# Kernel optimization log

Hardware: AMD Instinct MI355X
Metric: run time of the kernel (lower is better)

The kernel has to match this reference:

```python
import jax, jax.numpy as jnp
import numpy as np

# static config (matches init_kwargs)
E = 1280          # n_embed
L = 4             # n_layer
NH = 16           # n_heads
D = E // NH       # head_dim = 80
M = 5120          # n_mlp
O = 2048          # n_output_embed
MS = 2            # spatial_merge_size
NGPS = 48         # sqrt(num_position_embeddings)
GRID_T, GRID_H, GRID_W = 1, 32, 32
N_IMG = 2
SPP = GRID_T * GRID_H * GRID_W   # 1024 tokens per image
S = N_IMG * SPP                  # 2048 total tokens
H4 = E * MS * MS                 # merger hidden = 5120
IN_PATCH = 3 * 2 * 16 * 16       # 1536
DS_IDX = [1, 2]


def _ln(x, w, b, eps=1e-6):
    m = x.mean(-1, keepdims=True)
    v = ((x - m) ** 2).mean(-1, keepdims=True)
    return (x - m) / jnp.sqrt(v + eps) * w + b


def _pos_embed_interp(pos_emb):
    # bilinear interpolation of the 48x48 learned grid to GRID_HxGRID_W, per image
    hi = jnp.linspace(0.0, NGPS - 1.0, GRID_H)
    wi = jnp.linspace(0.0, NGPS - 1.0, GRID_W)
    hf = hi.astype(jnp.int32); wf = wi.astype(jnp.int32)
    hc = jnp.minimum(hf + 1, NGPS - 1); wc = jnp.minimum(wf + 1, NGPS - 1)
    dh = hi - hf; dw = wi - wf
    idx = [(hf[:, None] * NGPS + wf[None]).ravel(), (hf[:, None] * NGPS + wc[None]).ravel(),
           (hc[:, None] * NGPS + wf[None]).ravel(), (hc[:, None] * NGPS + wc[None]).ravel()]
    wts = [((1 - dh)[:, None] * (1 - dw)[None]).ravel(), ((1 - dh)[:, None] * dw[None]).ravel(),
           (dh[:, None] * (1 - dw)[None]).ravel(), (dh[:, None] * dw[None]).ravel()]
    pe = sum(pos_emb[i] * w[:, None] for i, w in zip(idx, wts))  # [h*w, E]
    pe = jnp.tile(pe, (GRID_T, 1))
    # spatial-merge permutation: (t, h/m, m, w/m, m) -> (t, h/m, w/m, m, m)
    pe = pe.reshape(GRID_T, GRID_H // MS, MS, GRID_W // MS, MS, E).transpose(0, 1, 3, 2, 4, 5).reshape(-1, E)
    return jnp.tile(pe, (N_IMG, 1))  # [S, E]


def _rotary_freqs():
    dim = D // 2  # VisionRotaryEmbedding dim = 40
    inv = 1.0 / (10000.0 ** (jnp.arange(0, dim, 2, dtype=jnp.float32) / dim))  # [D//4]
    hp = jnp.broadcast_to(jnp.arange(GRID_H)[:, None], (GRID_H, GRID_W))
    hp = hp.reshape(GRID_H // MS, MS, GRID_W // MS, MS).transpose(0, 2, 1, 3).ravel()
    wp = jnp.broadcast_to(jnp.arange(GRID_W)[None, :], (GRID_H, GRID_W))
    wp = wp.reshape(GRID_H // MS, MS, GRID_W // MS, MS).transpose(0, 2, 1, 3).ravel()
    pos = jnp.stack([hp, wp], -1)            # [h*w, 2]
    pos = jnp.tile(pos, (GRID_T, 1))
    pos = jnp.tile(pos, (N_IMG, 1))          # [S, 2]
    table = jnp.arange(max(GRID_H, GRID_W), dtype=jnp.float32)[:, None] * inv[None]  # [G, D//4]
    return table[pos].reshape(S, -1)         # [S, D//2] (h-freqs || w-freqs)


def _rope(t, cos, sin):
    # t: [S, NH, D]; cos/sin: [S, 1, D]; applied in float32 as in the source
    t1, t2 = jnp.split(t, 2, axis=-1)
    rot = jnp.concatenate([-t2, t1], -1)
    return (t.astype(jnp.float32) * cos + rot.astype(jnp.float32) * sin).astype(t.dtype)


def _attn(x, qkv_w, qkv_b, pw, pb, cos, sin, mask):
    qkv = (x @ qkv_w.T + qkv_b).reshape(S, 3, NH, D)
    q, k, v = qkv[:, 0], qkv[:, 1], qkv[:, 2]
    q = _rope(q, cos, sin)
    k = _rope(k, cos, sin)
    scores = jnp.einsum('shd,thd->hst', q, k) / np.sqrt(D).astype(np.float32) + mask
    p = jax.nn.softmax(scores.astype(jnp.float32), axis=-1).astype(q.dtype)
    o = jnp.einsum('hst,thd->shd', p, v).reshape(S, E)
    return o @ pw.T + pb


def _merger(x, ln_w, ln_b, f1w, f1b, f2w, f2b, post):
    if post:
        x = _ln(x.reshape(-1, H4), ln_w, ln_b)
    else:
        x = _ln(x, ln_w, ln_b).reshape(-1, H4)
    h = jax.nn.gelu(x @ f1w.T + f1b, approximate=False)  # nn.GELU() exact
    return h @ f2w.T + f2b


def setup_inputs() -> dict:
    key = jax.random.key(0)
    ks = iter(jax.random.split(key, 24))
    n = lambda s: jax.random.normal(next(ks), s, dtype=jnp.float32) * 0.02
    return {
        'x': jax.random.normal(next(ks), (S, IN_PATCH), dtype=jnp.float32),
        'patch_w': n((E, IN_PATCH)), 'patch_b': jnp.zeros((E,), jnp.float32),
        'pos_emb': n((NGPS * NGPS, E)),
        'ln1_w': jnp.ones((L, E), jnp.float32), 'ln1_b': jnp.zeros((L, E), jnp.float32),
        'ln2_w': jnp.ones((L, E), jnp.float32), 'ln2_b': jnp.zeros((L, E), jnp.float32),
        'qkv_w': n((L, 3 * E, E)), 'qkv_b': jnp.zeros((L, 3 * E), jnp.float32),
        'attn_proj_w': n((L, E, E)), 'attn_proj_b': jnp.zeros((L, E), jnp.float32),
        'fc1_w': n((L, M, E)), 'fc1_b': jnp.zeros((L, M), jnp.float32),
        'fc2_w': n((L, E, M)), 'fc2_b': jnp.zeros((L, E), jnp.float32),
        'm_ln_w': jnp.ones((E,), jnp.float32), 'm_ln_b': jnp.zeros((E,), jnp.float32),
        'm_fc1_w': n((H4, H4)), 'm_fc1_b': jnp.zeros((H4,), jnp.float32),
        'm_fc2_w': n((O, H4)), 'm_fc2_b': jnp.zeros((O,), jnp.float32),
        'ds_ln_w': jnp.ones((2, H4), jnp.float32), 'ds_ln_b': jnp.zeros((2, H4), jnp.float32),
        'ds_fc1_w': n((2, H4, H4)), 'ds_fc1_b': jnp.zeros((2, H4), jnp.float32),
        'ds_fc2_w': n((2, O, H4)), 'ds_fc2_b': jnp.zeros((2, O), jnp.float32),
    }


def reference(x, patch_w, patch_b, pos_emb, ln1_w, ln1_b, ln2_w, ln2_b,
              qkv_w, qkv_b, attn_proj_w, attn_proj_b, fc1_w, fc1_b, fc2_w, fc2_b,
              m_ln_w, m_ln_b, m_fc1_w, m_fc1_b, m_fc2_w, m_fc2_b,
              ds_ln_w, ds_ln_b, ds_fc1_w, ds_fc1_b, ds_fc2_w, ds_fc2_b):
    # patch embed (Conv3d with kernel==stride == per-patch linear)
    h = x @ patch_w.T + patch_b                      # [S, E]
    h = h + _pos_embed_interp(pos_emb)
    freqs = _rotary_freqs()                          # [S, D//2]
    cos = jnp.concatenate([jnp.cos(freqs)] * 2, -1)[:, None, :]  # [S,1,D]
    sin = jnp.concatenate([jnp.sin(freqs)] * 2, -1)[:, None, :]
    img = jnp.arange(S) // SPP                       # cu_seqlens block-diagonal mask
    mask = jnp.where(img[:, None] == img[None, :], 0.0, jnp.finfo(jnp.float32).min)
    ds_feats = []
    for l in range(L):
        h = h + _attn(_ln(h, ln1_w[l], ln1_b[l]), qkv_w[l], qkv_b[l],
                      attn_proj_w[l], attn_proj_b[l], cos, sin, mask)
        hn = _ln(h, ln2_w[l], ln2_b[l])
        h = h + (jax.nn.gelu(hn @ fc1_w[l].T + fc1_b[l], approximate=True) @ fc2_w[l].T + fc2_b[l])
        if l in DS_IDX:
            j = DS_IDX.index(l)
            ds_feats.append(_merger(h, ds_ln_w[j], ds_ln_b[j], ds_fc1_w[j], ds_fc1_b[j],
                                    ds_fc2_w[j], ds_fc2_b[j], post=True))
    main = _merger(h, m_ln_w, m_ln_b, m_fc1_w, m_fc1_b, m_fc2_w, m_fc2_b, post=False)
    return jnp.stack([main] + ds_feats, 0)           # [3, S//4, O]
```

## Files before the change

kernel.cpp:

```cpp
#include <hip/hip_runtime.h>
#include <hip/hip_bf16.h>
#include <cstdio>
#include <cstdint>

#define E_    1280
#define L_    4
#define NH_   16
#define D_    80
#define DP_   96
#define MLP_  5120
#define O_    2048
#define S_    2048
#define H4_   5120
#define INP_  1536

typedef __attribute__((ext_vector_type(4))) float f32x4;
typedef __attribute__((ext_vector_type(8))) short short8v;
typedef __attribute__((ext_vector_type(4))) short short4v;

__device__ __forceinline__ short f2bf(float f){
  uint32_t u = __float_as_uint(f);
  uint32_t r = (u + 0x7FFFu + ((u >> 16) & 1u)) >> 16;
  return (short)r;
}
__device__ __forceinline__ float bf2f(short s){
  return __uint_as_float(((uint32_t)(uint16_t)s) << 16);
}
__device__ __forceinline__ float gelu_tanh(float x){
  return 0.5f*x*(1.f + tanhf(0.7978845608028654f*(x + 0.044715f*x*x*x)));
}
__device__ __forceinline__ float gelu_erf(float x){
  return 0.5f*x*(1.f + erff(x*0.7071067811865476f));
}
__device__ __forceinline__ void token_hw(int t, int& hc, int& wc){
  hc = ((t>>1)&1) + ((t>>6)<<1);
  wc = (t&1)      + (((t>>2)&15)<<1);
}

__device__ __forceinline__ void gload16(const short* g, short* l){
  __builtin_amdgcn_global_load_lds((const __attribute__((address_space(1))) void*)g,
                                   (__attribute__((address_space(3))) void*)l, 16, 0, 0);
}

__global__ __launch_bounds__(256)
void cvt_k(const float* __restrict__ src, short* __restrict__ dst, long long n)
{
  const long long stride = (long long)gridDim.x*256*8;
  for (long long i = ((long long)blockIdx.x*256 + threadIdx.x)*8; i < n; i += stride){
    if (i + 8 <= n){
      float4 v0 = *(const float4*)(src+i);
      float4 v1 = *(const float4*)(src+i+4);
      short8v w;
      w[0]=f2bf(v0.x); w[1]=f2bf(v0.y); w[2]=f2bf(v0.z); w[3]=f2bf(v0.w);
      w[4]=f2bf(v1.x); w[5]=f2bf(v1.y); w[6]=f2bf(v1.z); w[7]=f2bf(v1.w);
      *(short8v*)(dst+i) = w;
    } else {
      for (long long j=i;j<n;j++) dst[j] = f2bf(src[j]);
    }
  }
}

struct Gemm2P {
  const short* A; const short* B; void* C;
  const float* bias;
  float* part;
  int lda, ldb, ldc, M, N, K;
  float scale;
  long long aOffH, aOffI, bOffH, bOffI, cOffH, cOffI;
  int nImg, kSplit;
};

template<int EPI, bool RES, bool CF32, bool SPLIT>
__global__ __launch_bounds__(256)
void gemm2_k(Gemm2P p)
{
  __shared__ short As[3][4096];
  __shared__ short Bs[3][4096];

  int z = blockIdx.z, ks = 0;
  if constexpr (SPLIT){ ks = z % p.kSplit; z /= p.kSplit; }
  const int hI = z / p.nImg, iI = z % p.nImg;
  const long long aB = (long long)hI*p.aOffH + (long long)iI*p.aOffI;
  const long long bB = (long long)hI*p.bOffH + (long long)iI*p.bOffI;
  const long long cB = (long long)hI*p.cOffH + (long long)iI*p.cOffI;

  const int nwg = gridDim.x*gridDim.y;
  const int orig = blockIdx.y*gridDim.x + blockIdx.x;
  const int q8 = nwg >> 3, r8 = nwg & 7;
  const int xcd = orig & 7, oidx = orig >> 3;
  const int wg = (xcd < r8 ? xcd*(q8+1) : r8*(q8+1) + (xcd-r8)*q8) + oidx;
  const int nt = wg % gridDim.x, mt = wg / gridDim.x;

  const int tid = threadIdx.x, lane = tid & 63, wv = tid >> 6;

  const int sr = lane >> 2;
  const int sc = (lane & 3) * 8;
  const int Kp  = SPLIT ? p.K / p.kSplit : p.K;
  const int kBeg = SPLIT ? ks * Kp : 0;
  int ra0 = mt*128 + (wv*2+0)*16 + sr; if (ra0 >= p.M) ra0 = p.M-1;
  int ra1 = mt*128 + (wv*2+1)*16 + sr; if (ra1 >= p.M) ra1 = p.M-1;
  int rb0 = nt*128 + (wv*2+0)*16 + sr; if (rb0 >= p.N) rb0 = p.N-1;
  int rb1 = nt*128 + (wv*2+1)*16 + sr; if (rb1 >= p.N) rb1 = p.N-1;
  const short* pa0 = p.A + aB + (long long)ra0*p.lda + sc + kBeg;
  const short* pa1 = p.A + aB + (long long)ra1*p.lda + sc + kBeg;
  const short* pb0 = p.B + bB + (long long)rb0*p.ldb + sc + kBeg;
  const short* pb1 = p.B + bB + (long long)rb1*p.ldb + sc + kBeg;
  const int so0 = (wv*2+0)*512;
  const int so1 = (wv*2+1)*512;

  const int fr = lane & 15, fo = (lane >> 4) * 8;
  const int wr = (wv >> 1) * 64, wc = (wv & 1) * 64;

  f32x4 acc[4][4] = {};

  auto stage = [&](int buf, int t){
    const int k0 = t << 5;
    gload16(pa0 + k0, &As[buf][so0]);
    gload16(pa1 + k0, &As[buf][so1]);
    gload16(pb0 + k0, &Bs[buf][so0]);
    gload16(pb1 + k0, &Bs[buf][so1]);
  };

  const int ntile = Kp >> 5;
  stage(0, 0);
  if (ntile > 1) stage(1, 1);
  for (int t = 0; t < ntile; t++){
    const int cur = t % 3;
    if (t + 1 < ntile) { asm volatile("s_waitcnt vmcnt(4)" ::: "memory"); }
    else               { asm volatile("s_waitcnt vmcnt(0)" ::: "memory"); }
    __builtin_amdgcn_s_barrier();
    asm volatile("" ::: "memory");
    short8v a[4], b[4];
    #pragma unroll
    for (int i=0;i<4;i++){
      a[i] = *(const short8v*)&As[cur][(wr + i*16 + fr)*32 + fo];
      b[i] = *(const short8v*)&Bs[cur][(wc + i*16 + fr)*32 + fo];
    }
    #pragma unroll
    for (int i=0;i<4;i++)
      #pragma unroll
      for (int j=0;j<4;j++)
        acc[i][j] = __builtin_amdgcn_mfma_f32_16x16x32_bf16(a[i], b[j], acc[i][j], 0, 0, 0);
    if (t + 2 < ntile) stage((t+2)%3, t+2);
  }

  #pragma unroll
  for (int i=0;i<4;i++){
    #pragma unroll
    for (int j=0;j<4;j++){
      #pragma unroll
      for (int r=0;r<4;r++){
        const int row = mt*128 + wr + i*16 + (lane>>4)*4 + r;
        const int col = nt*128 + wc + j*16 + fr;
        if (row < p.M && col < p.N){
          float v = acc[i][j][r];
          if constexpr (SPLIT){
            p.part[((long long)ks*p.M + row)*p.N + col] = v;
          } else {
            if (p.bias) v += p.bias[col];
            if constexpr (EPI==1) v = gelu_tanh(v);
            if constexpr (EPI==2) v = gelu_erf(v);
            if constexpr (EPI==3) v *= p.scale;
            const long long off = cB + (long long)row*p.ldc + col;
            if constexpr (RES)  v += ((const float*)p.C)[off];
            if constexpr (CF32) ((float*)p.C)[off] = v;
            else                ((short*)p.C)[off] = f2bf(v);
          }
        }
      }
    }
  }
}

template<int EPI, bool RES, bool CF32>
__global__ __launch_bounds__(256)
void reduce_k(const float* __restrict__ part, int kSplit, long long MN, int N,
              const float* __restrict__ bias, void* __restrict__ C)
{
  const long long i = ((long long)blockIdx.x*256 + threadIdx.x)*4;
  if (i >= MN) return;
  float4 s = *(const float4*)(part + i);
  for (int ks = 1; ks < kSplit; ks++){
    const float4 v = *(const float4*)(part + (long long)ks*MN + i);
    s.x += v.x; s.y += v.y; s.z += v.z; s.w += v.w;
  }
  if (bias){
    const int col = (int)(i % N);
    const float4 b = *(const float4*)(bias + col);
    s.x += b.x; s.y += b.y; s.z += b.z; s.w += b.w;
  }
  if constexpr (EPI==1){ s.x=gelu_tanh(s.x); s.y=gelu_tanh(s.y); s.z=gelu_tanh(s.z); s.w=gelu_tanh(s.w); }
  if constexpr (EPI==2){ s.x=gelu_erf(s.x);  s.y=gelu_erf(s.y);  s.z=gelu_erf(s.z);  s.w=gelu_erf(s.w); }
  if constexpr (RES){
    const float4 r = *(const float4*)((const float*)C + i);
    s.x += r.x; s.y += r.y; s.z += r.z; s.w += r.w;
  }
  if constexpr (CF32){
    *(float4*)((float*)C + i) = s;
  } else {
    short4v o; o[0]=f2bf(s.x); o[1]=f2bf(s.y); o[2]=f2bf(s.z); o[3]=f2bf(s.w);
    *(short4v*)((short*)C + i) = o;
  }
}

__global__ __launch_bounds__(256)
void fattn_k(const short* __restrict__ qh, const short* __restrict__ kh,
             const short* __restrict__ vt, short* __restrict__ o2)
{
  __shared__ short Ks[2][13312];
  __shared__ short Vs[2][12288];
  __shared__ short Ps[17408];

  const int qt = blockIdx.x, h = blockIdx.y, img = blockIdx.z;
  const int tid = threadIdx.x, lane = tid & 63, wv = tid >> 6;
  const int fr = lane & 15, fo = (lane >> 4) * 8, g = lane >> 4;
  const int wr = wv * 32;

  const short* qp = qh + ((long long)h*S_ + img*1024 + qt*128)*DP_;
  const short* kp = kh + ((long long)h*S_ + img*1024)*DP_;
  const short* vp = vt + ((long long)(h*2 + img))*80*1024;

  short8v q[2][3];
  #pragma unroll
  for (int i=0;i<2;i++)
    #pragma unroll
    for (int t3=0;t3<3;t3++)
      q[i][t3] = *(const short8v*)(qp + (long long)(wr + i*16 + fr)*DP_ + t3*32 + fo);

  int rK[7], cK[7], rV[6], cV[6];
  #pragma unroll
  for (int it=0; it<7; it++){
    const int o = it*4096 + tid*16;
    int r = o / 208, c = o % 208;
    if (c >= 192) c = 0;
    rK[it] = r; cK[it] = c >> 1;
  }
  #pragma unroll
  for (int it=0; it<6; it++){
    const int o = it*4096 + tid*16;
    int r = o / 304, c = o % 304;
    if (r >= 80){ r = 0; c = 0; }
    if (c >= 256) c = 0;
    rV[it] = r; cV[it] = c >> 1;
  }

  auto stage = [&](int b, int t){
    #pragma unroll
    for (int it=0; it<7; it++)
      if (it*4 + wv < 26)
        gload16(kp + (long long)(t*128 + rK[it])*DP_ + cK[it], &Ks[b][it*2048 + wv*512]);
    #pragma unroll
    for (int it=0; it<6; it++)
      gload16(vp + (long long)rV[it]*1024 + t*128 + cV[it], &Vs[b][it*2048 + wv*512]);
  };

  float m_[2][4], l_[2][4];
  f32x4 ao[2][5] = {};
  #pragma unroll
  for (int i=0;i<2;i++)
    #pragma unroll
    for (int r=0;r<4;r++){ m_[i][r] = -3.0e38f; l_[i][r] = 0.f; }

  stage(0, 0);
  __syncthreads();

  for (int t = 0; t < 8; t++){
    const int b = t & 1;
    if (t < 7) stage(b^1, t+1);

    f32x4 sc[2][8] = {};
    #pragma unroll
    for (int j=0;j<8;j++){
      #pragma unroll
      for (int t3=0;t3<3;t3++){
        const short8v kb = *(const short8v*)&Ks[b][(j*16+fr)*104 + t3*32 + fo];
        sc[0][j] = __builtin_amdgcn_mfma_f32_16x16x32_bf16(q[0][t3], kb, sc[0][j], 0,0,0);
        sc[1][j] = __builtin_amdgcn_mfma_f32_16x16x32_bf16(q[1][t3], kb, sc[1][j], 0,0,0);
      }
    }
    #pragma unroll
    for (int i=0;i<2;i++)
      #pragma unroll
      for (int j=0;j<8;j++)
        sc[i][j] *= 0.11180339887498949f;

    #pragma unroll
    for (int i=0;i<2;i++){
      #pragma unroll
      for (int r=0;r<4;r++){
        float mx = sc[i][0][r];
        #pragma unroll
        for (int j=1;j<8;j++) mx = fmaxf(mx, sc[i][j][r]);
        mx = fmaxf(mx, __shfl_xor(mx, 1, 64));
        mx = fmaxf(mx, __shfl_xor(mx, 2, 64));
        mx = fmaxf(mx, __shfl_xor(mx, 4, 64));
        mx = fmaxf(mx, __shfl_xor(mx, 8, 64));
        const float mn = fmaxf(m_[i][r], mx);
        const float al = __expf(m_[i][r] - mn);
        float ts = 0.f;
        #pragma unroll
        for (int j=0;j<8;j++){
          const float pv = __expf(sc[i][j][r] - mn);
          sc[i][j][r] = pv;
          ts += pv;
        }
        ts += __shfl_xor(ts, 1, 64);
        ts += __shfl_xor(ts, 2, 64);
        ts += __shfl_xor(ts, 4, 64);
        ts += __shfl_xor(ts, 8, 64);
        l_[i][r] = l_[i][r]*al + ts;
        m_[i][r] = mn;
        #pragma unroll
        for (int n=0;n<5;n++) ao[i][n][r] *= al;
        const int row = wr + i*16 + g*4 + r;
        #pragma unroll
        for (int j=0;j<8;j++) Ps[row*136 + j*16 + fr] = f2bf(sc[i][j][r]);
      }
    }

    #pragma unroll
    for (int t4=0;t4<4;t4++){
      short8v pa0 = *(const short8v*)&Ps[(wr + 0  + fr)*136 + t4*32 + fo];
      short8v pa1 = *(const short8v*)&Ps[(wr + 16 + fr)*136 + t4*32 + fo];
      #pragma unroll
      for (int n=0;n<5;n++){
        const short8v vb = *(const short8v*)&Vs[b][(n*16+fr)*152 + t4*32 + fo];
        ao[0][n] = __builtin_amdgcn_mfma_f32_16x16x32_bf16(pa0, vb, ao[0][n], 0,0,0);
        ao[1][n] = __builtin_amdgcn_mfma_f32_16x16x32_bf16(pa1, vb, ao[1][n], 0,0,0);
      }
    }
    __syncthreads();
  }

  short* op = o2 + ((long long)(img*1024 + qt*128))*E_ + h*80;
  #pragma unroll
  for (int i=0;i<2;i++){
    #pragma unroll
    for (int r=0;r<4;r++){
      const float inv = 1.f / l_[i][r];
      const int row = wr + i*16 + g*4 + r;
      #pragma unroll
      for (int n=0;n<5;n++)
        op[(long long)row*E_ + n*16 + fr] = f2bf(ao[i][n][r] * inv);
    }
  }
}

__global__ __launch_bounds__(256)
void ln_k(const float* __restrict__ X, const float* __restrict__ g, const float* __restrict__ bta,
          short* __restrict__ Y, int Cn)
{
  __shared__ float red[8];
  const int row = blockIdx.x;
  const float* x = X + (long long)row*Cn;
  short* y = Y + (long long)row*Cn;
  float s = 0.f, sq = 0.f;
  for (int c = threadIdx.x*4; c < Cn; c += 1024){
    float4 v = *(const float4*)(x + c);
    s  += v.x+v.y+v.z+v.w;
    sq += v.x*v.x+v.y*v.y+v.z*v.z+v.w*v.w;
  }
  #pragma unroll
  for (int m=32;m;m>>=1){ s += __shfl_xor(s,m,64); sq += __shfl_xor(sq,m,64); }
  const int wv = threadIdx.x>>6, lane = threadIdx.x&63;
  if (lane==0){ red[wv]=s; red[4+wv]=sq; }
  __syncthreads();
  s  = red[0]+red[1]+red[2]+red[3];
  sq = red[4]+red[5]+red[6]+red[7];
  const float mean = s / (float)Cn;
  const float var  = sq / (float)Cn - mean*mean;
  const float rs   = rsqrtf(var + 1e-6f);
  for (int c = threadIdx.x*4; c < Cn; c += 1024){
    float4 v  = *(const float4*)(x + c);
    float4 gw = *(const float4*)(g + c);
    float4 bw = *(const float4*)(bta + c);
    short4v o;
    o[0] = f2bf((v.x-mean)*rs*gw.x + bw.x);
    o[1] = f2bf((v.y-mean)*rs*gw.y + bw.y);
    o[2] = f2bf((v.z-mean)*rs*gw.z + bw.z);
    o[3] = f2bf((v.w-mean)*rs*gw.w + bw.w);
    *(short4v*)(y + c) = o;
  }
}

__global__ __launch_bounds__(256)
void rope_k(const short* __restrict__ qkv, short* __restrict__ qh,
            short* __restrict__ kh, short* __restrict__ vt)
{
  const int idx = blockIdx.x*256 + threadIdx.x;
  if (idx >= S_*NH_*40) return;
  const int d0 = idx % 40;
  const int h  = (idx / 40) % NH_;
  const int s  = idx / (40*NH_);
  const int t  = s & 1023, img = s >> 10;
  int hc, wc; token_hw(t, hc, wc);
  const int j  = d0 % 20;
  const float invf = exp2f(-0.66438561897747f * (float)j);
  const float pos  = (float)((d0 < 20) ? hc : wc);
  float sn, cs; sincosf(pos * invf, &sn, &cs);
  const short* base = qkv + (long long)s*3840 + h*80;
  const float q1 = bf2f(base[d0]),      q2 = bf2f(base[d0+40]);
  const float k1 = bf2f(base[1280+d0]), k2 = bf2f(base[1280+d0+40]);
  const long long qo = ((long long)h*S_ + s)*DP_;
  qh[qo + d0]    = f2bf(q1*cs - q2*sn);
  qh[qo + d0+40] = f2bf(q2*cs + q1*sn);
  kh[qo + d0]    = f2bf(k1*cs - k2*sn);
  kh[qo + d0+40] = f2bf(k2*cs + k1*sn);
  if (d0 < 16){ qh[qo + 80 + d0] = 0; kh[qo + 80 + d0] = 0; }
  const long long vo = (((long long)h*2 + img)*80)*1024 + t;
  vt[vo + (long long)d0*1024]      = base[2560+d0];
  vt[vo + (long long)(d0+40)*1024] = base[2560+d0+40];
}

__global__ __launch_bounds__(256)
void posadd_k(float* __restrict__ h, const float* __restrict__ pe)
{
  const int idx = blockIdx.x*256 + threadIdx.x;
  if (idx >= S_*(E_/4)) return;
  const int c4 = idx % (E_/4), s = idx / (E_/4);
  const int e = c4*4;
  const int t = s & 1023;
  int hc, wc; token_hw(t, hc, wc);
  const float hi = (float)hc * (47.f/31.f);
  const float wi = (float)wc * (47.f/31.f);
  int hf = (int)hi; float dh = hi - (float)hf; int h2 = min(hf+1, 47);
  int wf = (int)wi; float dw = wi - (float)wf; int w2 = min(wf+1, 47);
  const float w00=(1.f-dh)*(1.f-dw), w01=(1.f-dh)*dw, w10=dh*(1.f-dw), w11=dh*dw;
  const float4 a = *(const float4*)(pe + ((long long)(hf*48+wf))*E_ + e);
  const float4 b = *(const float4*)(pe + ((long long)(hf*48+w2))*E_ + e);
  const float4 c = *(const float4*)(pe + ((long long)(h2*48+wf))*E_ + e);
  const float4 d = *(const float4*)(pe + ((long long)(h2*48+w2))*E_ + e);
  float* out = h + (long long)s*E_ + e;
  float4 o = *(float4*)out;
  o.x += w00*a.x + w01*b.x + w10*c.x + w11*d.x;
  o.y += w00*a.y + w01*b.y + w10*c.y + w11*d.y;
  o.z += w00*a.z + w01*b.z + w10*c.z + w11*d.z;
  o.w += w00*a.w + w01*b.w + w10*c.w + w11*d.w;
  *(float4*)out = o;
}

static Gemm2P mk(const short* A, const short* B, void* C, const float* bias,
                 int lda, int ldb, int ldc, int M, int N, int K, float scale = 1.f)
{
  Gemm2P p{}; p.A=A; p.B=B; p.C=C; p.bias=bias; p.part=nullptr;
  p.lda=lda; p.ldb=ldb; p.ldc=ldc; p.M=M; p.N=N; p.K=K; p.scale=scale;
  p.aOffH=p.aOffI=p.bOffH=p.bOffI=p.cOffH=p.cOffI=0; p.nImg=1; p.kSplit=1;
  return p;
}

extern "C" void kernel_launch(void* const* d_in, const int* in_sizes, int n_in,
                              void* d_out, int out_size, void* d_ws, size_t ws_size,
                              hipStream_t stream)
{
  const float* x           = (const float*)d_in[0];
  const float* patch_w     = (const float*)d_in[1];
  const float* patch_b     = (const float*)d_in[2];
  const float* pos_emb     = (const float*)d_in[3];
  const float* ln1_w       = (const float*)d_in[4];
  const float* ln1_b       = (const float*)d_in[5];
  const float* ln2_w       = (const float*)d_in[6];
  const float* ln2_b       = (const float*)d_in[7];
  const float* qkv_w       = (const float*)d_in[8];
  const float* qkv_b       = (const float*)d_in[9];
  const float* attn_proj_w = (const float*)d_in[10];
  const float* attn_proj_b = (const float*)d_in[11];
  const float* fc1_w       = (const float*)d_in[12];
  const float* fc1_b       = (const float*)d_in[13];
  const float* fc2_w       = (const float*)d_in[14];
  const float* fc2_b       = (const float*)d_in[15];
  const float* m_ln_w      = (const float*)d_in[16];
  const float* m_ln_b      = (const float*)d_in[17];
  const float* m_fc1_w     = (const float*)d_in[18];
  const float* m_fc1_b     = (const float*)d_in[19];
  const float* m_fc2_w     = (const float*)d_in[20];
  const float* m_fc2_b     = (const float*)d_in[21];
  const float* ds_ln_w     = (const float*)d_in[22];
  const float* ds_ln_b     = (const float*)d_in[23];
  const float* ds_fc1_w    = (const float*)d_in[24];
  const float* ds_fc1_b    = (const float*)d_in[25];
  const float* ds_fc2_w    = (const float*)d_in[26];
  const float* ds_fc2_b    = (const float*)d_in[27];
  float* out = (float*)d_out;

  char* wsp = (char*)d_ws;
  auto alloc = [&](size_t bytes)->char*{
    char* p = wsp; wsp += (bytes + 255) & ~(size_t)255; return p;
  };
  float* h    = (float*)alloc((size_t)S_*E_*4);
  short* qkvb = (short*)alloc((size_t)S_*3840*2);
  short* aln  = (short*)alloc((size_t)S_*E_*2);
  short* qh   = (short*)alloc((size_t)NH_*S_*DP_*2);
  short* kh   = (short*)alloc((size_t)NH_*S_*DP_*2 + 4096);
  short* vt   = (short*)alloc((size_t)NH_*2*D_*1024*2 + 4096);
  float* part = (float*)alloc((size_t)48*1024*1024);
  short* o2   = (short*)alloc((size_t)S_*E_*2);
  short* ffn  = (short*)alloc((size_t)S_*MLP_*2);
  short* xb    = (short*)alloc((size_t)S_*INP_*2);
  short* pwB   = (short*)alloc((size_t)E_*INP_*2);
  short* qkvwB = (short*)alloc((size_t)L_*3840*E_*2);
  short* prwB  = (short*)alloc((size_t)L_*E_*E_*2);
  short* f1wB  = (short*)alloc((size_t)L_*MLP_*E_*2);
  short* f2wB  = (short*)alloc((size_t)L_*E_*MLP_*2);
  short* mf1B  = (short*)alloc((size_t)H4_*H4_*2);
  short* mf2B  = (short*)alloc((size_t)O_*H4_*2);
  short* df1B  = (short*)alloc((size_t)2*H4_*H4_*2);
  short* df2B  = (short*)alloc((size_t)2*O_*H4_*2);
  size_t need = (size_t)(wsp - (char*)d_ws);
  if (need > ws_size){
    fprintf(stderr, "kernel_launch: ws too small: need %zu have %zu\n", need, ws_size);
    return;
  }

  const dim3 B256(256);
  auto cvt = [&](const float* src, short* dst, long long n){
    unsigned blk = (unsigned)min((long long)8192, (n/8 + 255)/256);
    cvt_k<<<blk, B256, 0, stream>>>(src, dst, n);
  };
  cvt(x, xb, (long long)S_*INP_);
  cvt(patch_w, pwB, (long long)E_*INP_);
  cvt(qkv_w, qkvwB, (long long)L_*3840*E_);
  cvt(attn_proj_w, prwB, (long long)L_*E_*E_);
  cvt(fc1_w, f1wB, (long long)L_*MLP_*E_);
  cvt(fc2_w, f2wB, (long long)L_*E_*MLP_);
  cvt(m_fc1_w, mf1B, (long long)H4_*H4_);
  cvt(m_fc2_w, mf2B, (long long)O_*H4_);
  cvt(ds_fc1_w, df1B, (long long)2*H4_*H4_);
  cvt(ds_fc2_w, df2B, (long long)2*O_*H4_);

  auto G = [](int M, int N, int ks = 1){
    return dim3((unsigned)((N+127)/128), (unsigned)((M+127)/128), (unsigned)ks);
  };
  auto RG = [](long long MN){ return dim3((unsigned)((MN/4 + 255)/256)); };

  { Gemm2P pp = mk(xb, pwB, h, nullptr, INP_, INP_, E_, S_, E_, INP_);
    pp.part = part; pp.kSplit = 4;
    gemm2_k<0,false,true,true><<<G(S_,E_,4),B256,0,stream>>>(pp);
    reduce_k<0,false,true><<<RG((long long)S_*E_),B256,0,stream>>>(part, 4, (long long)S_*E_, E_, patch_b, h); }
  posadd_k<<<(S_*(E_/4)+255)/256, B256, 0, stream>>>(h, pos_emb);

  for (int l = 0; l < L_; l++){
    ln_k<<<S_, B256, 0, stream>>>(h, ln1_w + l*E_, ln1_b + l*E_, aln, E_);
    { Gemm2P pp = mk(aln, qkvwB + (size_t)l*3840*E_, qkvb, qkv_b + l*3840, E_, E_, 3840, S_, 3840, E_);
      gemm2_k<0,false,false,false><<<G(S_,3840),B256,0,stream>>>(pp); }
    rope_k<<<(S_*NH_*40+255)/256, B256, 0, stream>>>(qkvb, qh, kh, vt);
    fattn_k<<<dim3(8,16,2), B256, 0, stream>>>(qh, kh, vt, o2);
    { Gemm2P pp = mk(o2, prwB + (size_t)l*E_*E_, h, nullptr, E_, E_, E_, S_, E_, E_);
      pp.part = part; pp.kSplit = 4;
      gemm2_k<0,false,true,true><<<G(S_,E_,4),B256,0,stream>>>(pp);
      reduce_k<0,true,true><<<RG((long long)S_*E_),B256,0,stream>>>(part, 4, (long long)S_*E_, E_, attn_proj_b + l*E_, h); }

    ln_k<<<S_, B256, 0, stream>>>(h, ln2_w + l*E_, ln2_b + l*E_, aln, E_);
    { Gemm2P pp = mk(aln, f1wB + (size_t)l*MLP_*E_, ffn, fc1_b + l*MLP_, E_, E_, MLP_, S_, MLP_, E_);
      gemm2_k<1,false,false,false><<<G(S_,MLP_),B256,0,stream>>>(pp); }
    { Gemm2P pp = mk(ffn, f2wB + (size_t)l*E_*MLP_, h, nullptr, MLP_, MLP_, E_, S_, E_, MLP_);
      pp.part = part; pp.kSplit = 4;
      gemm2_k<0,false,true,true><<<G(S_,E_,4),B256,0,stream>>>(pp);
      reduce_k<0,true,true><<<RG((long long)S_*E_),B256,0,stream>>>(part, 4, (long long)S_*E_, E_, fc2_b + l*E_, h); }

    if (l == 1 || l == 2){
      const int j = l - 1;
      ln_k<<<512, B256, 0, stream>>>(h, ds_ln_w + (size_t)j*H4_, ds_ln_b + (size_t)j*H4_, aln, H4_);
      { Gemm2P pp = mk(aln, df1B + (size_t)j*H4_*H4_, ffn, nullptr, H4_, H4_, H4_, 512, H4_, H4_);
        pp.part = part; pp.kSplit = 4;
        gemm2_k<0,false,false,true><<<G(512,H4_,4),B256,0,stream>>>(pp);
        reduce_k<2,false,false><<<RG((long long)512*H4_),B256,0,stream>>>(part, 4, (long long)512*H4_, H4_, ds_fc1_b + (size_t)j*H4_, ffn); }
      { Gemm2P pp = mk(ffn, df2B + (size_t)j*O_*H4_, out + (size_t)(1+j)*512*O_, nullptr, H4_, H4_, O_, 512, O_, H4_);
        pp.part = part; pp.kSplit = 8;
        gemm2_k<0,false,true,true><<<G(512,O_,8),B256,0,stream>>>(pp);
        reduce_k<0,false,true><<<RG((long long)512*O_),B256,0,stream>>>(part, 8, (long long)512*O_, O_, ds_fc2_b + (size_t)j*O_, out + (size_t)(1+j)*512*O_); }
    }
  }

  ln_k<<<S_, B256, 0, stream>>>(h, m_ln_w, m_ln_b, aln, E_);
  { Gemm2P pp = mk(aln, mf1B, ffn, nullptr, H4_, H4_, H4_, 512, H4_, H4_);
    pp.part = part; pp.kSplit = 4;
    gemm2_k<0,false,false,true><<<G(512,H4_,4),B256,0,stream>>>(pp);
    reduce_k<2,false,false><<<RG((long long)512*H4_),B256,0,stream>>>(part, 4, (long long)512*H4_, H4_, m_fc1_b, ffn); }
  { Gemm2P pp = mk(ffn, mf2B, out, nullptr, H4_, H4_, O_, 512, O_, H4_);
    pp.part = part; pp.kSplit = 8;
    gemm2_k<0,false,true,true><<<G(512,O_,8),B256,0,stream>>>(pp);
    reduce_k<0,false,true><<<RG((long long)512*O_),B256,0,stream>>>(part, 8, (long long)512*O_, O_, m_fc2_b, out); }
}
```

Baseline: 1.635 ms.

## Fuse split-K reduce with layernorm, use bf16 partials, rework attention and conversion

Split-K GEMMs now write bf16 partial sums instead of fp32, halving partial-buffer traffic. A new redln kernel fuses the residual reduce with the following layernorm, which removes separate ln launches. Weight conversion becomes a single batched launch instead of ten. Flash attention drops its LDS staging of K/V and reads them straight from global with one wave per 16 query rows, launching twice as many blocks. The GEMM prefetch is issued before the MFMAs. Rounding the partials to bf16 risks a loss of accuracy in the residual stream.

Result: slower. 1.779 ms (+8.8%).

```diff
diff --git a/kernel.cpp b/kernel.cpp
--- a/kernel.cpp
+++ b/kernel.cpp
@@ -42,28 +42,32 @@
                                    (__attribute__((address_space(3))) void*)l, 16, 0, 0);
 }
 
-__global__ __launch_bounds__(256)
-void cvt_k(const float* __restrict__ src, short* __restrict__ dst, long long n)
+struct CvtSeg { const float* src; short* dst; long long n; };
+struct CvtP { CvtSeg s[10]; long long tot; };
+
+__global__ __launch_bounds__(256)
+void cvtall_k(CvtP p)
 {
   const long long stride = (long long)gridDim.x*256*8;
-  for (long long i = ((long long)blockIdx.x*256 + threadIdx.x)*8; i < n; i += stride){
-    if (i + 8 <= n){
-      float4 v0 = *(const float4*)(src+i);
-      float4 v1 = *(const float4*)(src+i+4);
-      short8v w;
-      w[0]=f2bf(v0.x); w[1]=f2bf(v0.y); w[2]=f2bf(v0.z); w[3]=f2bf(v0.w);
-      w[4]=f2bf(v1.x); w[5]=f2bf(v1.y); w[6]=f2bf(v1.z); w[7]=f2bf(v1.w);
-      *(short8v*)(dst+i) = w;
-    } else {
-      for (long long j=i;j<n;j++) dst[j] = f2bf(src[j]);
-    }
+  for (long long i = ((long long)blockIdx.x*256 + threadIdx.x)*8; i < p.tot; i += stride){
+    long long off = i; int si = 0;
+    #pragma unroll
+    for (int k=0;k<9;k++){ if (off >= p.s[si].n){ off -= p.s[si].n; si++; } }
+    const float* src = p.s[si].src + off;
+    short* dst = p.s[si].dst + off;
+    float4 v0 = *(const float4*)(src);
+    float4 v1 = *(const float4*)(src+4);
+    short8v w;
+    w[0]=f2bf(v0.x); w[1]=f2bf(v0.y); w[2]=f2bf(v0.z); w[3]=f2bf(v0.w);
+    w[4]=f2bf(v1.x); w[5]=f2bf(v1.y); w[6]=f2bf(v1.z); w[7]=f2bf(v1.w);
+    *(short8v*)dst = w;
   }
 }
 
 struct Gemm2P {
   const short* A; const short* B; void* C;
   const float* bias;
-  float* part;
+  short* part;
   int lda, ldb, ldc, M, N, K;
   float scale;
   long long aOffH, aOffI, bOffH, bOffI, cOffH, cOffI;
@@ -136,12 +140,12 @@
       a[i] = *(const short8v*)&As[cur][(wr + i*16 + fr)*32 + fo];
       b[i] = *(const short8v*)&Bs[cur][(wc + i*16 + fr)*32 + fo];
     }
+    if (t + 2 < ntile) stage((t+2)%3, t+2);
     #pragma unroll
     for (int i=0;i<4;i++)
       #pragma unroll
       for (int j=0;j<4;j++)
         acc[i][j] = __builtin_amdgcn_mfma_f32_16x16x32_bf16(a[i], b[j], acc[i][j], 0, 0, 0);
-    if (t + 2 < ntile) stage((t+2)%3, t+2);
   }
 
   #pragma unroll
@@ -155,7 +159,7 @@
         if (row < p.M && col < p.N){
           float v = acc[i][j][r];
           if constexpr (SPLIT){
-            p.part[((long long)ks*p.M + row)*p.N + col] = v;
+            p.part[((long long)ks*p.M + row)*p.N + col] = f2bf(v);
           } else {
             if (p.bias) v += p.bias[col];
             if constexpr (EPI==1) v = gelu_tanh(v);
@@ -174,32 +178,98 @@
 
 template<int EPI, bool RES, bool CF32>
 __global__ __launch_bounds__(256)
-void reduce_k(const float* __restrict__ part, int kSplit, long long MN, int N,
+void reduce_k(const short* __restrict__ part, int kSplit, long long MN, int N,
               const float* __restrict__ bias, void* __restrict__ C)
 {
-  const long long i = ((long long)blockIdx.x*256 + threadIdx.x)*4;
+  const long long i = ((long long)blockIdx.x*256 + threadIdx.x)*8;
   if (i >= MN) return;
-  float4 s = *(const float4*)(part + i);
+  float v[8];
+  { short8v pv = *(const short8v*)(part + i);
+    #pragma unroll
+    for (int e=0;e<8;e++) v[e] = bf2f(pv[e]); }
   for (int ks = 1; ks < kSplit; ks++){
-    const float4 v = *(const float4*)(part + (long long)ks*MN + i);
-    s.x += v.x; s.y += v.y; s.z += v.z; s.w += v.w;
+    short8v pv = *(const short8v*)(part + (long long)ks*MN + i);
+    #pragma unroll
+    for (int e=0;e<8;e++) v[e] += bf2f(pv[e]);
   }
   if (bias){
     const int col = (int)(i % N);
-    const float4 b = *(const float4*)(bias + col);
-    s.x += b.x; s.y += b.y; s.z += b.z; s.w += b.w;
-  }
-  if constexpr (EPI==1){ s.x=gelu_tanh(s.x); s.y=gelu_tanh(s.y); s.z=gelu_tanh(s.z); s.w=gelu_tanh(s.w); }
-  if constexpr (EPI==2){ s.x=gelu_erf(s.x);  s.y=gelu_erf(s.y);  s.z=gelu_erf(s.z);  s.w=gelu_erf(s.w); }
+    #pragma unroll
+    for (int e=0;e<8;e++) v[e] += bias[col+e];
+  }
+  #pragma unroll
+  for (int e=0;e<8;e++){
+    if constexpr (EPI==1) v[e] = gelu_tanh(v[e]);
+    if constexpr (EPI==2) v[e] = gelu_erf(v[e]);
+  }
   if constexpr (RES){
-    const float4 r = *(const float4*)((const float*)C + i);
-    s.x += r.x; s.y += r.y; s.z += r.z; s.w += r.w;
+    const float* cp = (const float*)C + i;
+    #pragma unroll
+    for (int e=0;e<8;e++) v[e] += cp[e];
   }
   if constexpr (CF32){
-    *(float4*)((float*)C + i) = s;
+    float4 o0 = {v[0],v[1],v[2],v[3]}, o1 = {v[4],v[5],v[6],v[7]};
+    *(float4*)((float*)C + i) = o0;
+    *(float4*)((float*)C + i + 4) = o1;
   } else {
-    short4v o; o[0]=f2bf(s.x); o[1]=f2bf(s.y); o[2]=f2bf(s.z); o[3]=f2bf(s.w);
-    *(short4v*)((short*)C + i) = o;
+    short8v o;
+    #pragma unroll
+    for (int e=0;e<8;e++) o[e] = f2bf(v[e]);
+    *(short8v*)((short*)C + i) = o;
+  }
+}
+
+__global__ __launch_bounds__(256)
+void redln_k(const short* __restrict__ part, long long MN, const float* __restrict__ bias,
+             float* __restrict__ h, const float* __restrict__ lnw, const float* __restrict__ lnb,
+             short* __restrict__ aln)
+{
+  __shared__ float red[8];
+  const int row = blockIdx.x, tid = threadIdx.x;
+  float4 vals[2];
+  float s = 0.f, sq = 0.f;
+  #pragma unroll
+  for (int it=0; it<2; it++){
+    const int c = tid*4 + it*1024;
+    if (c < E_){
+      float4 v = *(const float4*)(h + (long long)row*E_ + c);
+      const float4 b = *(const float4*)(bias + c);
+      v.x += b.x; v.y += b.y; v.z += b.z; v.w += b.w;
+      #pragma unroll
+      for (int ks=0; ks<4; ks++){
+        short4v pv = *(const short4v*)(part + (long long)ks*MN + (long long)row*E_ + c);
+        v.x += bf2f(pv[0]); v.y += bf2f(pv[1]); v.z += bf2f(pv[2]); v.w += bf2f(pv[3]);
+      }
+      *(float4*)(h + (long long)row*E_ + c) = v;
+      vals[it] = v;
+      s  += v.x+v.y+v.z+v.w;
+      sq += v.x*v.x+v.y*v.y+v.z*v.z+v.w*v.w;
+    }
+  }
+  #pragma unroll
+  for (int m=32;m;m>>=1){ s += __shfl_xor(s,m,64); sq += __shfl_xor(sq,m,64); }
+  const int wv = tid>>6, lane = tid&63;
+  if (lane==0){ red[wv]=s; red[4+wv]=sq; }
+  __syncthreads();
+  s  = red[0]+red[1]+red[2]+red[3];
+  sq = red[4]+red[5]+red[6]+red[7];
+  const float mean = s / (float)E_;
+  const float var  = sq / (float)E_ - mean*mean;
+  const float rs   = rsqrtf(var + 1e-6f);
+  #pragma unroll
+  for (int it=0; it<2; it++){
+    const int c = tid*4 + it*1024;
+    if (c < E_){
+      const float4 v = vals[it];
+      const float4 gw = *(const float4*)(lnw + c);
+      const float4 bw = *(const float4*)(lnb + c);
+      short4v o;
+      o[0] = f2bf((v.x-mean)*rs*gw.x + bw.x);
+      o[1] = f2bf((v.y-mean)*rs*gw.y + bw.y);
+      o[2] = f2bf((v.z-mean)*rs*gw.z + bw.z);
+      o[3] = f2bf((v.w-mean)*rs*gw.w + bw.w);
+      *(short4v*)(aln + (long long)row*E_ + c) = o;
+    }
   }
 }
 
@@ -207,142 +277,92 @@
 void fattn_k(const short* __restrict__ qh, const short* __restrict__ kh,
              const short* __restrict__ vt, short* __restrict__ o2)
 {
-  __shared__ short Ks[2][13312];
-  __shared__ short Vs[2][12288];
-  __shared__ short Ps[17408];
+  __shared__ short Ps[4][16*136];
 
   const int qt = blockIdx.x, h = blockIdx.y, img = blockIdx.z;
   const int tid = threadIdx.x, lane = tid & 63, wv = tid >> 6;
   const int fr = lane & 15, fo = (lane >> 4) * 8, g = lane >> 4;
-  const int wr = wv * 32;
-
-  const short* qp = qh + ((long long)h*S_ + img*1024 + qt*128)*DP_;
+
+  const short* qp = qh + ((long long)h*S_ + img*1024 + qt*64 + wv*16)*DP_;
   const short* kp = kh + ((long long)h*S_ + img*1024)*DP_;
   const short* vp = vt + ((long long)(h*2 + img))*80*1024;
-
-  short8v q[2][3];
-  #pragma unroll
-  for (int i=0;i<2;i++)
-    #pragma unroll
-    for (int t3=0;t3<3;t3++)
-      q[i][t3] = *(const short8v*)(qp + (long long)(wr + i*16 + fr)*DP_ + t3*32 + fo);
-
-  int rK[7], cK[7], rV[6], cV[6];
-  #pragma unroll
-  for (int it=0; it<7; it++){
-    const int o = it*4096 + tid*16;
-    int r = o / 208, c = o % 208;
-    if (c >= 192) c = 0;
-    rK[it] = r; cK[it] = c >> 1;
-  }
-  #pragma unroll
-  for (int it=0; it<6; it++){
-    const int o = it*4096 + tid*16;
-    int r = o / 304, c = o % 304;
-    if (r >= 80){ r = 0; c = 0; }
-    if (c >= 256) c = 0;
-    rV[it] = r; cV[it] = c >> 1;
-  }
-
-  auto stage = [&](int b, int t){
-    #pragma unroll
-    for (int it=0; it<7; it++)
-      if (it*4 + wv < 26)
-        gload16(kp + (long long)(t*128 + rK[it])*DP_ + cK[it], &Ks[b][it*2048 + wv*512]);
-    #pragma unroll
-    for (int it=0; it<6; it++)
-      gload16(vp + (long long)rV[it]*1024 + t*128 + cV[it], &Vs[b][it*2048 + wv*512]);
-  };
-
-  float m_[2][4], l_[2][4];
-  f32x4 ao[2][5] = {};
-  #pragma unroll
-  for (int i=0;i<2;i++)
-    #pragma unroll
-    for (int r=0;r<4;r++){ m_[i][r] = -3.0e38f; l_[i][r] = 0.f; }
-
-  stage(0, 0);
-  __syncthreads();
+  short* Pw = &Ps[wv][0];
+
+  short8v q[3];
+  #pragma unroll
+  for (int t3=0;t3<3;t3++)
+    q[t3] = *(const short8v*)(qp + (long long)fr*DP_ + t3*32 + fo);
+
+  float m_[4], l_[4];
+  f32x4 ao[5] = {};
+  #pragma unroll
+  for (int r=0;r<4;r++){ m_[r] = -3.0e38f; l_[r] = 0.f; }
 
   for (int t = 0; t < 8; t++){
-    const int b = t & 1;
-    if (t < 7) stage(b^1, t+1);
-
-    f32x4 sc[2][8] = {};
+    f32x4 sc[8] = {};
     #pragma unroll
     for (int j=0;j<8;j++){
       #pragma unroll
       for (int t3=0;t3<3;t3++){
-        const short8v kb = *(const short8v*)&Ks[b][(j*16+fr)*104 + t3*32 + fo];
-        sc[0][j] = __builtin_amdgcn_mfma_f32_16x16x32_bf16(q[0][t3], kb, sc[0][j], 0,0,0);
-        sc[1][j] = __builtin_amdgcn_mfma_f32_16x16x32_bf16(q[1][t3], kb, sc[1][j], 0,0,0);
+        const short8v kb = *(const short8v*)(kp + (long long)(t*128 + j*16 + fr)*DP_ + t3*32 + fo);
+        sc[j] = __builtin_amdgcn_mfma_f32_16x16x32_bf16(q[t3], kb, sc[j], 0,0,0);
       }
     }
     #pragma unroll
-    for (int i=0;i<2;i++)
-      #pragma unroll
-      for (int j=0;j<8;j++)
-        sc[i][j] *= 0.11180339887498949f;
-
-    #pragma unroll
-    for (int i=0;i<2;i++){
-      #pragma unroll
-      for (int r=0;r<4;r++){
-        float mx = sc[i][0][r];
-        #pragma unroll
-        for (int j=1;j<8;j++) mx = fmaxf(mx, sc[i][j][r]);
-        mx = fmaxf(mx, __shfl_xor(mx, 1, 64));
-        mx = fmaxf(mx, __shfl_xor(mx, 2, 64));
-        mx = fmaxf(mx, __shfl_xor(mx, 4, 64));
-        mx = fmaxf(mx, __shfl_xor(mx, 8, 64));
-        const float mn = fmaxf(m_[i][r], mx);
-        const float al = __expf(m_[i][r] - mn);
-        float ts = 0.f;
-        #pragma unroll
-        for (int j=0;j<8;j++){
-          const float pv = __expf(sc[i][j][r] - mn);
-          sc[i][j][r] = pv;
-          ts += pv;
-        }
-        ts += __shfl_xor(ts, 1, 64);
-        ts += __shfl_xor(ts, 2, 64);
-        ts += __shfl_xor(ts, 4, 64);
-        ts += __shfl_xor(ts, 8, 64);
-        l_[i][r] = l_[i][r]*al + ts;
-        m_[i][r] = mn;
-        #pragma unroll
-        for (int n=0;n<5;n++) ao[i][n][r] *= al;
-        const int row = wr + i*16 + g*4 + r;
-        #pragma unroll
-        for (int j=0;j<8;j++) Ps[row*136 + j*16 + fr] = f2bf(sc[i][j][r]);
+    for (int j=0;j<8;j++) sc[j] *= 0.11180339887498949f;
+
+    #pragma unroll
+    for (int r=0;r<4;r++){
+      float mx = sc[0][r];
+      #pragma unroll
+      for (int j=1;j<8;j++) mx = fmaxf(mx, sc[j][r]);
+      mx = fmaxf(mx, __shfl_xor(mx, 1, 64));
+      mx = fmaxf(mx, __shfl_xor(mx, 2, 64));
+      mx = fmaxf(mx, __shfl_xor(mx, 4, 64));
+      mx = fmaxf(mx, __shfl_xor(mx, 8, 64));
+      const float mn = fmaxf(m_[r], mx);
+      const float al = __expf(m_[r] - mn);
+      float ts = 0.f;
+      #pragma unroll
+      for (int j=0;j<8;j++){
+        const float pv = __expf(sc[j][r] - mn);
+        sc[j][r] = pv;
+        ts += pv;
       }
-    }
+      ts += __shfl_xor(ts, 1, 64);
+      ts += __shfl_xor(ts, 2, 64);
+      ts += __shfl_xor(ts, 4, 64);
+      ts += __shfl_xor(ts, 8, 64);
+      l_[r] = l_[r]*al + ts;
+      m_[r] = mn;
+      #pragma unroll
+      for (int n=0;n<5;n++) ao[n][r] *= al;
+      const int prow = g*4 + r;
+      #pragma unroll
+      for (int j=0;j<8;j++) Pw[prow*136 + j*16 + fr] = f2bf(sc[j][r]);
+    }
+    asm volatile("s_waitcnt lgkmcnt(0)" ::: "memory");
+    __builtin_amdgcn_sched_barrier(0);
 
     #pragma unroll
     for (int t4=0;t4<4;t4++){
-      short8v pa0 = *(const short8v*)&Ps[(wr + 0  + fr)*136 + t4*32 + fo];
-      short8v pa1 = *(const short8v*)&Ps[(wr + 16 + fr)*136 + t4*32 + fo];
+      const short8v pa = *(const short8v*)&Pw[fr*136 + t4*32 + fo];
       #pragma unroll
       for (int n=0;n<5;n++){
-        const short8v vb = *(const short8v*)&Vs[b][(n*16+fr)*152 + t4*32 + fo];
-        ao[0][n] = __builtin_amdgcn_mfma_f32_16x16x32_bf16(pa0, vb, ao[0][n], 0,0,0);
-        ao[1][n] = __builtin_amdgcn_mfma_f32_16x16x32_bf16(pa1, vb, ao[1][n], 0,0,0);
+        const short8v vb = *(const short8v*)(vp + (long long)(n*16 + fr)*1024 + t*128 + t4*32 + fo);
+        ao[n] = __builtin_amdgcn_mfma_f32_16x16x32_bf16(pa, vb, ao[n], 0,0,0);
       }
     }
-    __syncthreads();
-  }
-
-  short* op = o2 + ((long long)(img*1024 + qt*128))*E_ + h*80;
-  #pragma unroll
-  for (int i=0;i<2;i++){
-    #pragma unroll
-    for (int r=0;r<4;r++){
-      const float inv = 1.f / l_[i][r];
-      const int row = wr + i*16 + g*4 + r;
-      #pragma unroll
-      for (int n=0;n<5;n++)
-        op[(long long)row*E_ + n*16 + fr] = f2bf(ao[i][n][r] * inv);
-    }
+  }
+
+  short* op = o2 + ((long long)(img*1024 + qt*64 + wv*16))*E_ + h*80;
+  #pragma unroll
+  for (int r=0;r<4;r++){
+    const float inv = 1.f / l_[r];
+    const int row = g*4 + r;
+    #pragma unroll
+    for (int n=0;n<5;n++)
+      op[(long long)row*E_ + n*16 + fr] = f2bf(ao[n][r] * inv);
   }
 }
 
@@ -492,7 +512,7 @@
   short* qh   = (short*)alloc((size_t)NH_*S_*DP_*2);
   short* kh   = (short*)alloc((size_t)NH_*S_*DP_*2 + 4096);
   short* vt   = (short*)alloc((size_t)NH_*2*D_*1024*2 + 4096);
-  float* part = (float*)alloc((size_t)48*1024*1024);
+  short* part = (short*)alloc((size_t)24*1024*1024);
   short* o2   = (short*)alloc((size_t)S_*E_*2);
   short* ffn  = (short*)alloc((size_t)S_*MLP_*2);
   short* xb    = (short*)alloc((size_t)S_*INP_*2);
@@ -510,57 +530,61 @@
     fprintf(stderr, "kernel_launch: ws too small: need %zu have %zu\n", need, ws_size);
     return;
   }
+  short* dsln = qkvb;
 
   const dim3 B256(256);
-  auto cvt = [&](const float* src, short* dst, long long n){
-    unsigned blk = (unsigned)min((long long)8192, (n/8 + 255)/256);
-    cvt_k<<<blk, B256, 0, stream>>>(src, dst, n);
-  };
-  cvt(x, xb, (long long)S_*INP_);
-  cvt(patch_w, pwB, (long long)E_*INP_);
-  cvt(qkv_w, qkvwB, (long long)L_*3840*E_);
-  cvt(attn_proj_w, prwB, (long long)L_*E_*E_);
-  cvt(fc1_w, f1wB, (long long)L_*MLP_*E_);
-  cvt(fc2_w, f2wB, (long long)L_*E_*MLP_);
-  cvt(m_fc1_w, mf1B, (long long)H4_*H4_);
-  cvt(m_fc2_w, mf2B, (long long)O_*H4_);
-  cvt(ds_fc1_w, df1B, (long long)2*H4_*H4_);
-  cvt(ds_fc2_w, df2B, (long long)2*O_*H4_);
+
+  { CvtP cp{};
+    cp.s[0] = { x,         xb,    (long long)S_*INP_ };
+    cp.s[1] = { patch_w,   pwB,   (long long)E_*INP_ };
+    cp.s[2] = { qkv_w,     qkvwB, (long long)L_*3840*E_ };
+    cp.s[3] = { attn_proj_w, prwB, (long long)L_*E_*E_ };
+    cp.s[4] = { fc1_w,     f1wB,  (long long)L_*MLP_*E_ };
+    cp.s[5] = { fc2_w,     f2wB,  (long long)L_*E_*MLP_ };
+    cp.s[6] = { m_fc1_w,   mf1B,  (long long)H4_*H4_ };
+    cp.s[7] = { m_fc2_w,   mf2B,  (long long)O_*H4_ };
+    cp.s[8] = { ds_fc1_w,  df1B,  (long long)2*H4_*H4_ };
+    cp.s[9] = { ds_fc2_w,  df2B,  (long long)2*O_*H4_ };
+    cp.tot = 0;
+    for (int i=0;i<10;i++) cp.tot += cp.s[i].n;
+    cvtall_k<<<2048, B256, 0, stream>>>(cp); }
 
   auto G = [](int M, int N, int ks = 1){
     return dim3((unsigned)((N+127)/128), (unsigned)((M+127)/128), (unsigned)ks);
   };
-  auto RG = [](long long MN){ return dim3((unsigned)((MN/4 + 255)/256)); };
+  auto RG = [](long long MN){ return dim3((unsigned)((MN/8 + 255)/256)); };
 
   { Gemm2P pp = mk(xb, pwB, h, nullptr, INP_, INP_, E_, S_, E_, INP_);
     pp.part = part; pp.kSplit = 4;
     gemm2_k<0,false,true,true><<<G(S_,E_,4),B256,0,stream>>>(pp);
     reduce_k<0,false,true><<<RG((long long)S_*E_),B256,0,stream>>>(part, 4, (long long)S_*E_, E_, patch_b, h); }
   posadd_k<<<(S_*(E_/4)+255)/256, B256, 0, stream>>>(h, pos_emb);
+  ln_k<<<S_, B256, 0, stream>>>(h, ln1_w, ln1_b, aln, E_);
 
   for (int l = 0; l < L_; l++){
-    ln_k<<<S_, B256, 0, stream>>>(h, ln1_w + l*E_, ln1_b + l*E_, aln, E_);
     { Gemm2P pp = mk(aln, qkvwB + (size_t)l*3840*E_, qkvb, qkv_b + l*3840, E_, E_, 3840, S_, 3840, E_);
       gemm2_k<0,false,false,false><<<G(S_,3840),B256,0,stream>>>(pp); }
     rope_k<<<(S_*NH_*40+255)/256, B256, 0, stream>>>(qkvb, qh, kh, vt);
-    fattn_k<<<dim3(8,16,2), B256, 0, stream>>>(qh, kh, vt, o2);
-    { Gemm2P pp = mk(o2, prwB + (size_t)l*E_*E_, h, nullptr, E_, E_, E_, S_, E_, E_);
+    fattn_k<<<dim3(16,16,2), B256, 0, stream>>>(qh, kh, vt, o2);
+    { Gemm2P pp = mk(o2, prwB + (size_t)l*E_*E_, nullptr, nullptr, E_, E_, E_, S_, E_, E_);
       pp.part = part; pp.kSplit = 4;
       gemm2_k<0,false,true,true><<<G(S_,E_,4),B256,0,stream>>>(pp);
-      reduce_k<0,true,true><<<RG((long long)S_*E_),B256,0,stream>>>(part, 4, (long long)S_*E_, E_, attn_proj_b + l*E_, h); }
-
-    ln_k<<<S_, B256, 0, stream>>>(h, ln2_w + l*E_, ln2_b + l*E_, aln, E_);
+      redln_k<<<S_, B256, 0, stream>>>(part, (long long)S_*E_, attn_proj_b + l*E_,
+                                       h, ln2_w + l*E_, ln2_b + l*E_, aln); }
+
     { Gemm2P pp = mk(aln, f1wB + (size_t)l*MLP_*E_, ffn, fc1_b + l*MLP_, E_, E_, MLP_, S_, MLP_, E_);
       gemm2_k<1,false,false,false><<<G(S_,MLP_),B256,0,stream>>>(pp); }
-    { Gemm2P pp = mk(ffn, f2wB + (size_t)l*E_*MLP_, h, nullptr, MLP_, MLP_, E_, S_, E_, MLP_);
+    { Gemm2P pp = mk(ffn, f2wB + (size_t)l*E_*MLP_, nullptr, nullptr, MLP_, MLP_, E_, S_, E_, MLP_);
       pp.part = part; pp.kSplit = 4;
       gemm2_k<0,false,true,true><<<G(S_,E_,4),B256,0,stream>>>(pp);
-      reduce_k<0,true,true><<<RG((long long)S_*E_),B256,0,stream>>>(part, 4, (long long)S_*E_, E_, fc2_b + l*E_, h); }
+      const float* nw = (l < 3) ? (ln1_w + (l+1)*E_) : m_ln_w;
+      const float* nb = (l < 3) ? (ln1_b + (l+1)*E_) : m_ln_b;
+      redln_k<<<S_, B256, 0, stream>>>(part, (long long)S_*E_, fc2_b + l*E_, h, nw, nb, aln); }
 
     if (l == 1 || l == 2){
       const int j = l - 1;
-      ln_k<<<512, B256, 0, stream>>>(h, ds_ln_w + (size_t)j*H4_, ds_ln_b + (size_t)j*H4_, aln, H4_);
-      { Gemm2P pp = mk(aln, df1B + (size_t)j*H4_*H4_, ffn, nullptr, H4_, H4_, H4_, 512, H4_, H4_);
+      ln_k<<<512, B256, 0, stream>>>(h, ds_ln_w + (size_t)j*H4_, ds_ln_b + (size_t)j*H4_, dsln, H4_);
+      { Gemm2P pp = mk(dsln, df1B + (size_t)j*H4_*H4_, ffn, nullptr, H4_, H4_, H4_, 512, H4_, H4_);
         pp.part = part; pp.kSplit = 4;
         gemm2_k<0,false,false,true><<<G(512,H4_,4),B256,0,stream>>>(pp);
         reduce_k<2,false,false><<<RG((long long)512*H4_),B256,0,stream>>>(part, 4, (long long)512*H4_, H4_, ds_fc1_b + (size_t)j*H4_, ffn); }
@@ -571,7 +595,6 @@
     }
   }
 
-  ln_k<<<S_, B256, 0, stream>>>(h, m_ln_w, m_ln_b, aln, E_);
   { Gemm2P pp = mk(aln, mf1B, ffn, nullptr, H4_, H4_, H4_, 512, H4_, H4_);
     pp.part = part; pp.kSplit = 4;
     gemm2_k<0,false,false,true><<<G(512,H4_,4),B256,0,stream>>>(pp);
```
